# Kernel optimization log

Hardware: AMD Instinct MI355X
Metric: run time of the kernel (lower is better)

## Reference

```python
import jax, jax.numpy as jnp
import numpy as np

B, L, N, C = 16, 96, 1024, 3
EMB, GRAP, OUT, NLAYER = 64, 16, 12, 2


def setup_inputs() -> dict:
    key = jax.random.key(0)
    ks = jax.random.split(key, 16)
    s = 0.1
    return {
        "history_data": jax.random.normal(ks[0], (B, L, N, C), jnp.float32),
        # row-stochastic graph (normalized adjacency buffer)
        "adj": jax.nn.softmax(jax.random.normal(ks[1], (N, N), jnp.float32), axis=-1),
        "Wv0": jax.random.normal(ks[2], (C, EMB), jnp.float32) * s,
        "Wv1": jax.random.normal(ks[3], (EMB, EMB), jnp.float32) * s,
        "bv": jnp.zeros((NLAYER, EMB), jnp.float32),
        "E": jax.random.normal(ks[4], (NLAYER, N, EMB), jnp.float32) * s,
        "Wq": jax.random.normal(ks[5], (NLAYER, EMB, EMB), jnp.float32) * s,
        "Wk": jax.random.normal(ks[6], (NLAYER, EMB, EMB), jnp.float32) * s,
        "Eg1": jax.random.normal(ks[7], (NLAYER, N, GRAP), jnp.float32) * s,
        "Eg2": jax.random.normal(ks[8], (NLAYER, N, GRAP), jnp.float32) * s,
        "Wmix": jax.random.normal(ks[9], (NLAYER, 3, EMB, EMB), jnp.float32) * s,
        "bmix": jnp.zeros((NLAYER, EMB), jnp.float32),
        "Wgates": jax.random.normal(ks[10], (NLAYER, 4, EMB, EMB), jnp.float32) * s,
        "bgates": jnp.zeros((NLAYER, 4, EMB), jnp.float32),
        "Wdec": jax.random.normal(ks[11], (OUT, NLAYER, EMB), jnp.float32) * s,
        "bdec": jnp.zeros((OUT,), jnp.float32),
        "Wout": jax.random.normal(ks[12], (OUT, OUT), jnp.float32) * s,
        "bout": jnp.zeros((OUT,), jnp.float32),
    }


def reference(history_data, adj, Wv0, Wv1, bv, E, Wq, Wk, Eg1, Eg2,
              Wmix, bmix, Wgates, bgates, Wdec, bdec, Wout, bout):
    # GinAR forward (inference: dropout = identity, lay_norm unused in original forward).
    emb = Wv1.shape[0]
    inv = 1.0 / jnp.sqrt(jnp.float32(emb))
    x = history_data  # (B, L, N, in)
    finals = []
    for z in range(Wmix.shape[0]):
        Wv = Wv0 if z == 0 else Wv1
        # interpolation attention over variables (nodes), shared across time/batch
        q = E[z] @ Wq[z]
        k = E[z] @ Wk[z]
        attn = jax.nn.softmax((q @ k.T) * inv, axis=-1)                 # (N, N)
        # adaptive learned graph
        adp = jax.nn.softmax(jax.nn.relu(Eg1[z] @ Eg2[z].T), axis=-1)    # (N, N)
        bz, Wm, bm, Wg, bgz = bv[z], Wmix[z], bmix[z], Wgates[z], bgates[z]

        def step(ct, xt, Wv=Wv, attn=attn, adp=adp, bz=bz, Wm=Wm, bm=bm, Wg=Wg, bgz=bgz):
            v = xt @ Wv + bz                                # (B, N, emb)
            h = jnp.einsum('mn,bne->bme', attn, v)          # variable interpolation
            hg = (jnp.einsum('mn,bne->bme', adj, h) @ Wm[0]
                  + jnp.einsum('mn,bne->bme', adp, h) @ Wm[1]
                  + h @ Wm[2] + bm)                         # adaptive graph conv
            gates = jnp.einsum('bne,kef->kbnf', hg, Wg) + bgz[:, None, None, :]
            f = jax.nn.sigmoid(gates[0])
            i = jax.nn.sigmoid(gates[1])
            g = jnp.tanh(gates[2])
            o = jax.nn.sigmoid(gates[3])
            ct = f * ct + i * g
            ht = o * jnp.tanh(ct)
            return ct, ht

        ct0 = jnp.zeros((x.shape[0], x.shape[2], emb), x.dtype)
        _, hts = jax.lax.scan(step, ct0, jnp.moveaxis(x, 1, 0))  # (L, B, N, emb)
        x = jnp.moveaxis(hts, 0, 1)                              # (B, L, N, emb)
        finals.append(x[:, -1])                                  # last step -> (B, N, emb)
    final = jnp.stack(finals, axis=1)                            # (B, layers, N, emb)
    # decoder Conv2d(layer_num -> out_len, kernel (1, emb)) == contraction over (layer, emb)
    dec = jnp.einsum('blne,ole->bon', final, Wdec) + bdec[None, :, None]
    # 1x1 output conv
    out = jnp.einsum('bpn,op->bon', dec, Wout) + bout[None, :, None]
    return out  # (B, out_len, N)
```

## Files before the change

kernel.cpp:

```cpp
#include <hip/hip_runtime.h>
#include <hip/hip_bf16.h>

#define B_ 16
#define L_ 96
#define N_ 1024
#define EMB_ 64

typedef __hip_bfloat16 bf16;
typedef __attribute__((ext_vector_type(4))) float f32x4;
typedef __attribute__((ext_vector_type(8))) short s16x8;

__global__ __launch_bounds__(256) void gemm_nn(
    const float* __restrict__ A, const float* __restrict__ Bm, float* __restrict__ C,
    int M, int N, int K, int lda, int ldb, int ldc, const float* __restrict__ bias)
{
    __shared__ float As[64][17];
    __shared__ __align__(16) float Bs[16][64];
    const int tid = threadIdx.x;
    const int tx = tid & 15, ty = tid >> 4;
    const int row0 = blockIdx.y * 64, col0 = blockIdx.x * 64;
    float acc[4][4] = {};
    const int ak = tid & 15, ar = tid >> 4;
    const int bc = tid & 63, bk = tid >> 6;
    for (int k0 = 0; k0 < K; k0 += 16) {
#pragma unroll
        for (int i = 0; i < 4; ++i) {
            int r = ar + i * 16;
            int gr = row0 + r, gk = k0 + ak;
            As[r][ak] = (gr < M && gk < K) ? A[(size_t)gr * lda + gk] : 0.f;
        }
#pragma unroll
        for (int i = 0; i < 4; ++i) {
            int kk = bk + i * 4;
            int gk = k0 + kk, gc = col0 + bc;
            Bs[kk][bc] = (gk < K && gc < N) ? Bm[(size_t)gk * ldb + gc] : 0.f;
        }
        __syncthreads();
#pragma unroll
        for (int kk = 0; kk < 16; ++kk) {
            float4 b4 = *reinterpret_cast<const float4*>(&Bs[kk][tx * 4]);
            float a0 = As[ty * 4 + 0][kk];
            float a1 = As[ty * 4 + 1][kk];
            float a2 = As[ty * 4 + 2][kk];
            float a3 = As[ty * 4 + 3][kk];
            acc[0][0] += a0 * b4.x; acc[0][1] += a0 * b4.y; acc[0][2] += a0 * b4.z; acc[0][3] += a0 * b4.w;
            acc[1][0] += a1 * b4.x; acc[1][1] += a1 * b4.y; acc[1][2] += a1 * b4.z; acc[1][3] += a1 * b4.w;
            acc[2][0] += a2 * b4.x; acc[2][1] += a2 * b4.y; acc[2][2] += a2 * b4.z; acc[2][3] += a2 * b4.w;
            acc[3][0] += a3 * b4.x; acc[3][1] += a3 * b4.y; acc[3][2] += a3 * b4.z; acc[3][3] += a3 * b4.w;
        }
        __syncthreads();
    }
#pragma unroll
    for (int i = 0; i < 4; ++i) {
        int gr = row0 + ty * 4 + i;
        if (gr >= M) continue;
#pragma unroll
        for (int j = 0; j < 4; ++j) {
            int gc = col0 + tx * 4 + j;
            if (gc >= N) continue;
            float v = acc[i][j];
            if (bias) v += bias[gc];
            C[(size_t)gr * ldc + gc] = v;
        }
    }
}

__global__ __launch_bounds__(256) void gemm_nt(
    const float* __restrict__ A, const float* __restrict__ Bm, float* __restrict__ C,
    int N, int K, float alpha)
{
    __shared__ float As[64][65];
    __shared__ float Bs[64][65];
    const int tid = threadIdx.x;
    const int row0 = blockIdx.y * 64, col0 = blockIdx.x * 64;
    for (int idx = tid; idx < 64 * K; idx += 256) {
        int r = idx / K, c = idx % K;
        As[r][c] = A[(size_t)(row0 + r) * K + c];
        Bs[r][c] = Bm[(size_t)(col0 + r) * K + c];
    }
    __syncthreads();
    const int tx = tid & 15, ty = tid >> 4;
    float acc[4][4] = {};
    for (int c = 0; c < K; ++c) {
        float a[4], b[4];
#pragma unroll
        for (int i = 0; i < 4; ++i) a[i] = As[ty * 4 + i][c];
#pragma unroll
        for (int j = 0; j < 4; ++j) b[j] = Bs[tx * 4 + j][c];
#pragma unroll
        for (int i = 0; i < 4; ++i)
#pragma unroll
            for (int j = 0; j < 4; ++j) acc[i][j] += a[i] * b[j];
    }
#pragma unroll
    for (int i = 0; i < 4; ++i)
#pragma unroll
        for (int j = 0; j < 4; ++j)
            C[(size_t)(row0 + ty * 4 + i) * N + col0 + tx * 4 + j] = alpha * acc[i][j];
}

__global__ __launch_bounds__(256) void row_softmax(
    const float* __restrict__ in, float* __restrict__ out32, int os32,
    bf16* __restrict__ out16, int os16, int relu)
{
    const float* rp = in + (size_t)blockIdx.x * N_;
    const int tid = threadIdx.x;
    float v[4];
#pragma unroll
    for (int j = 0; j < 4; ++j) {
        float x = rp[tid + 256 * j];
        if (relu) x = fmaxf(x, 0.f);
        v[j] = x;
    }
    float m = fmaxf(fmaxf(v[0], v[1]), fmaxf(v[2], v[3]));
#pragma unroll
    for (int off = 32; off > 0; off >>= 1) m = fmaxf(m, __shfl_xor(m, off));
    __shared__ float red[4], red2[4];
    int w = tid >> 6;
    if ((tid & 63) == 0) red[w] = m;
    __syncthreads();
    m = fmaxf(fmaxf(red[0], red[1]), fmaxf(red[2], red[3]));
    float s = 0.f;
#pragma unroll
    for (int j = 0; j < 4; ++j) { v[j] = __expf(v[j] - m); s += v[j]; }
#pragma unroll
    for (int off = 32; off > 0; off >>= 1) s += __shfl_xor(s, off);
    if ((tid & 63) == 0) red2[w] = s;
    __syncthreads();
    s = red2[0] + red2[1] + red2[2] + red2[3];
    float inv = 1.f / s;
#pragma unroll
    for (int j = 0; j < 4; ++j) {
        float r = v[j] * inv;
        if (out32) out32[(size_t)blockIdx.x * os32 + tid + 256 * j] = r;
        if (out16) out16[(size_t)blockIdx.x * os16 + tid + 256 * j] = __float2bfloat16(r);
    }
}

__global__ __launch_bounds__(256) void transpose_f2b(
    const float* __restrict__ in, bf16* __restrict__ out)
{
    __shared__ float t[64][65];
    const int cx = blockIdx.x, cy = blockIdx.y;
    const int tid = threadIdx.x;
#pragma unroll
    for (int k = 0; k < 16; ++k) {
        int idx = k * 256 + tid;
        int r = idx >> 6, c = idx & 63;
        t[r][c] = in[(size_t)(cy * 64 + r) * 1024 + cx * 64 + c];
    }
    __syncthreads();
#pragma unroll
    for (int k = 0; k < 16; ++k) {
        int idx = k * 256 + tid;
        int r = idx >> 6, c = idx & 63;
        out[(size_t)(cx * 64 + r) * 1024 + cy * 64 + c] = __float2bfloat16(t[c][r]);
    }
}

__global__ __launch_bounds__(256) void wgct_kernel(const float* __restrict__ Wg,
                                                   bf16* __restrict__ WgcT)
{
    int i = blockIdx.x * 256 + threadIdx.x;
    int g = i >> 12, e = (i >> 6) & 63, f = i & 63;
    WgcT[(((size_t)g * 64 + f) << 6) + e] = __float2bfloat16(Wg[i]);
}

__global__ __launch_bounds__(256) void wvc1t_kernel(const float* __restrict__ Wvc1,
                                                    bf16* __restrict__ WT)
{
    int i = blockIdx.x * 256 + threadIdx.x;
    int row = i >> 6, f = i & 63;
    float v = 0.f;
    if (row < 192) { int kp = row >> 6, e = row & 63; v = Wvc1[kp * 4096 + f * 64 + e]; }
    WT[i] = __float2bfloat16(v);
}

__global__ __launch_bounds__(256) void f2b_kernel(const float* __restrict__ in,
                                                  bf16* __restrict__ out, int n)
{
    int i = blockIdx.x * 256 + threadIdx.x;
    if (i < n) out[i] = __float2bfloat16(in[i]);
}

__global__ __launch_bounds__(256) void bias_kernel(
    const float* __restrict__ bvz, const float* __restrict__ Wmz, const float* __restrict__ bmz,
    const float* __restrict__ Wgz, const float* __restrict__ bgz, float* __restrict__ bgconst)
{
    __shared__ float bconst[64];
    const int tid = threadIdx.x;
    if (tid < 64) {
        float s = bmz[tid];
        for (int kp = 0; kp < 3; ++kp)
            for (int f = 0; f < 64; ++f) s += bvz[f] * Wmz[kp * 4096 + f * 64 + tid];
        bconst[tid] = s;
    }
    __syncthreads();
    int g = tid >> 6, fo = tid & 63;
    float s = bgz[g * 64 + fo];
    for (int e = 0; e < 64; ++e) s += bconst[e] * Wgz[g * 4096 + e * 64 + fo];
    bgconst[tid] = s;
}

__global__ __launch_bounds__(256) void wbig_kernel(
    const float* __restrict__ Wvc0, const float* __restrict__ Wg0, bf16* __restrict__ WbigT)
{
    const int tid = threadIdx.x;
    const int g = tid >> 6, fo = tid & 63;
    float v[9];
#pragma unroll
    for (int q = 0; q < 9; ++q) {
        const int kp = q / 3, c = q % 3;
        float s = 0.f;
        for (int e = 0; e < 64; ++e)
            s += Wvc0[kp * 192 + c * 64 + e] * Wg0[g * 4096 + e * 64 + fo];
        v[q] = s;
    }
#pragma unroll
    for (int i = 0; i < 32; ++i)
        WbigT[(size_t)tid * 32 + i] = __float2bfloat16(i < 9 ? v[i] : 0.f);
}

__global__ __launch_bounds__(256) void xt_build(
    const float* __restrict__ hist, bf16* __restrict__ XT, int l0, int LC)
{
    __shared__ float xs[3][1024];
    const int lb = blockIdx.x;
    const int l = lb >> 4, b = lb & 15;
    const int tid = threadIdx.x;
    const float* xp = hist + ((size_t)b * L_ + (l0 + l)) * N_ * 3;
    for (int i = tid; i < 3072; i += 256) xs[i % 3][i / 3] = xp[i];
    __syncthreads();
#pragma unroll
    for (int c = 0; c < 3; ++c)
#pragma unroll
        for (int q = 0; q < 4; ++q) {
            int n = q * 256 + tid;
            XT[((size_t)lb * 3 + c) * 1024 + n] = __float2bfloat16(xs[c][n]);
        }
}

__device__ __forceinline__ void gload16(const bf16* g, bf16* l)
{
    __builtin_amdgcn_global_load_lds((const __attribute__((address_space(1))) void*)g,
                                     (__attribute__((address_space(3))) void*)l, 16, 0, 0);
}

template <int OUT_BF16, int REMAP>
__global__ __launch_bounds__(256) void gemm_mfma(
    const bf16* __restrict__ A, const bf16* __restrict__ BT, void* __restrict__ Cp,
    int M, int N, int K, int lda, int ldb, int ldc,
    const float* __restrict__ bias, int Nmask)
{
    __shared__ __align__(16) bf16 As[128 * 64];
    __shared__ __align__(16) bf16 Bs[128 * 64];
    const int tid = threadIdx.x;
    const int lane = tid & 63, w = tid >> 6;
    const int wr = w >> 1, wc = w & 1;
    const int row0 = blockIdx.y * 128, col0 = blockIdx.x * 128;
    if (REMAP == 1) BT += (size_t)blockIdx.z * 64;
    if (REMAP == 2) A += (size_t)blockIdx.z * 1024;

    f32x4 acc[4][4];
#pragma unroll
    for (int i = 0; i < 4; ++i)
#pragma unroll
        for (int j = 0; j < 4; ++j) acc[i][j] = (f32x4){0.f, 0.f, 0.f, 0.f};

    const int srow = w * 32 + (lane >> 3);
    const int scolsw = ((lane & 7) ^ (lane >> 3)) * 8;

    for (int k0 = 0; k0 < K; k0 += 64) {
#pragma unroll
        for (int i = 0; i < 4; ++i) {
            gload16(A + (size_t)(row0 + srow + i * 8) * lda + k0 + scolsw,
                    &As[(w * 32 + i * 8) * 64]);
            gload16(BT + (size_t)(col0 + srow + i * 8) * ldb + k0 + scolsw,
                    &Bs[(w * 32 + i * 8) * 64]);
        }
        __syncthreads();
#pragma unroll
        for (int kk = 0; kk < 64; kk += 32) {
            s16x8 af[4], bfr[4];
            const int ko = (kk + (lane >> 4) * 8) ^ ((lane & 7) << 3);
#pragma unroll
            for (int mi = 0; mi < 4; ++mi)
                af[mi] = *(const s16x8*)&As[(wr * 64 + mi * 16 + (lane & 15)) * 64 + ko];
#pragma unroll
            for (int ni = 0; ni < 4; ++ni)
                bfr[ni] = *(const s16x8*)&Bs[(wc * 64 + ni * 16 + (lane & 15)) * 64 + ko];
#pragma unroll
            for (int mi = 0; mi < 4; ++mi)
#pragma unroll
                for (int ni = 0; ni < 4; ++ni)
                    acc[mi][ni] = __builtin_amdgcn_mfma_f32_16x16x32_bf16(
                        af[mi], bfr[ni], acc[mi][ni], 0, 0, 0);
        }
        __syncthreads();
    }

    if (REMAP == 1) {
        bf16* outb = (bf16*)Cp + (size_t)blockIdx.z * (64 * 3072);
#pragma unroll
        for (int mi = 0; mi < 4; ++mi) {
            const int gr = row0 + wr * 64 + mi * 16 + (lane >> 4) * 4;
#pragma unroll
            for (int ni = 0; ni < 4; ++ni) {
                const int gc = col0 + wc * 64 + ni * 16 + (lane & 15);
#pragma unroll
                for (int j = 0; j < 4; ++j) {
                    const int r = gr + j;
                    if (r >= Nmask) continue;
                    outb[(size_t)(r & 63) * 3072 + (r >> 6) * 1024 + gc] =
                        __float2bfloat16(acc[mi][ni][j]);
                }
            }
        }
        return;
    }
    if (REMAP == 2) {
        bf16* outb = (bf16*)Cp;
        const int kpoff = blockIdx.z * 3;
#pragma unroll
        for (int mi = 0; mi < 4; ++mi) {
            const int gr = row0 + wr * 64 + mi * 16 + (lane >> 4) * 4;
#pragma unroll
            for (int ni = 0; ni < 4; ++ni) {
                const int gc = col0 + wc * 64 + ni * 16 + (lane & 15);
                if (gc >= Nmask) continue;
                const int dstc = (gc / 3) * 32 + kpoff + gc % 3;
#pragma unroll
                for (int j = 0; j < 4; ++j)
                    outb[(size_t)(gr + j) * ldc + dstc] = __float2bfloat16(acc[mi][ni][j]);
            }
        }
        return;
    }

#pragma unroll
    for (int mi = 0; mi < 4; ++mi) {
        const int gr = row0 + wr * 64 + mi * 16 + (lane >> 4) * 4;
#pragma unroll
        for (int ni = 0; ni < 4; ++ni) {
            const int gc = col0 + wc * 64 + ni * 16 + (lane & 15);
            if (gc >= Nmask) continue;
            const float bb = bias ? bias[gc] : 0.f;
#pragma unroll
            for (int j = 0; j < 4; ++j) {
                float v = acc[mi][ni][j] + bb;
                if (OUT_BF16)
                    ((bf16*)Cp)[(size_t)(gr + j) * ldc + gc] = __float2bfloat16(v);
                else
                    ((float*)Cp)[(size_t)(gr + j) * ldc + gc] = v;
            }
        }
    }
}

__global__ __launch_bounds__(512) void gemm_pipe(
    const bf16* __restrict__ A, const bf16* __restrict__ BT, bf16* __restrict__ C,
    int N, int K)
{
    __shared__ __align__(16) bf16 lds[8 * 8192];
    const int tid = threadIdx.x;
    const int lane = tid & 63, w = tid >> 6;
    const int wm = w >> 2, wn = w & 3, bh = wn >> 1;
    const int row0 = blockIdx.y * 256, col0 = blockIdx.x * 256;

    const int strow = tid >> 3;
    const int srck  = ((tid & 7) ^ ((tid >> 3) & 7)) << 3;
    const int e7 = lane & 7, fs = lane >> 4, a15 = lane & 15;

    int aoff0[8], boff0[4];
#pragma unroll
    for (int mi = 0; mi < 8; ++mi)
        aoff0[mi] = (mi * 16 + a15) * 64 + ((fs ^ e7) << 3);
#pragma unroll
    for (int ni = 0; ni < 4; ++ni)
        boff0[ni] = ((wn & 1) * 64 + ni * 16 + a15) * 64 + ((fs ^ e7) << 3);

    auto stage = [&](int mat, int half, int kt) {
        bf16* dst = &lds[(size_t)((((kt & 1) << 1) | mat) * 2 + half) * 8192 + w * 512];
        const bf16* src = (mat ? BT + (size_t)col0 * K : A + (size_t)row0 * K)
                          + (size_t)(half * 128) * K + kt * 64 + srck;
        gload16(src + (size_t)strow * K, dst);
        gload16(src + (size_t)(64 + strow) * K, dst + 4096);
    };

    f32x4 acc[8][4];
#pragma unroll
    for (int i = 0; i < 8; ++i)
#pragma unroll
        for (int j = 0; j < 4; ++j) acc[i][j] = (f32x4){0.f, 0.f, 0.f, 0.f};

    s16x8 b0, b1, b2, b3;

#define MF_(a, mi) { \
    acc[mi][0] = __builtin_amdgcn_mfma_f32_16x16x32_bf16(a, b0, acc[mi][0], 0, 0, 0); \
    acc[mi][1] = __builtin_amdgcn_mfma_f32_16x16x32_bf16(a, b1, acc[mi][1], 0, 0, 0); \
    acc[mi][2] = __builtin_amdgcn_mfma_f32_16x16x32_bf16(a, b2, acc[mi][2], 0, 0, 0); \
    acc[mi][3] = __builtin_amdgcn_mfma_f32_16x16x32_bf16(a, b3, acc[mi][3], 0, 0, 0); }

#define PH_(d, kh, g, DOB, STG) { \
    const bf16* Ab = &lds[((d) * 4 + wm) * 8192]; \
    const bf16* Bb = &lds[((d) * 4 + 2 + bh) * 8192]; \
    if (DOB) { \
        b0 = *(const s16x8*)&Bb[boff0[0] ^ ((kh) * 32)]; \
        b1 = *(const s16x8*)&Bb[boff0[1] ^ ((kh) * 32)]; \
        b2 = *(const s16x8*)&Bb[boff0[2] ^ ((kh) * 32)]; \
        b3 = *(const s16x8*)&Bb[boff0[3] ^ ((kh) * 32)]; \
    } \
    s16x8 a0 = *(const s16x8*)&Ab[aoff0[(g) * 4 + 0] ^ ((kh) * 32)]; \
    s16x8 a1 = *(const s16x8*)&Ab[aoff0[(g) * 4 + 1] ^ ((kh) * 32)]; \
    s16x8 a2 = *(const s16x8*)&Ab[aoff0[(g) * 4 + 2] ^ ((kh) * 32)]; \
    s16x8 a3 = *(const s16x8*)&Ab[aoff0[(g) * 4 + 3] ^ ((kh) * 32)]; \
    STG; \
    __builtin_amdgcn_s_barrier(); \
    asm volatile("s_waitcnt lgkmcnt(0)" ::: "memory"); \
    __builtin_amdgcn_sched_barrier(0); \
    __builtin_amdgcn_s_setprio(1); \
    MF_(a0, (g) * 4 + 0); MF_(a1, (g) * 4 + 1); \
    MF_(a2, (g) * 4 + 2); MF_(a3, (g) * 4 + 3); \
    __builtin_amdgcn_s_setprio(0); \
    __builtin_amdgcn_s_barrier(); }

    const int NT = K >> 6;
    stage(0, 0, 0); stage(0, 1, 0); stage(1, 0, 0); stage(1, 1, 0);
    stage(0, 0, 1);

    for (int i = 0; i < NT / 2; ++i) {
        const int kt = 2 * i;
        asm volatile("s_waitcnt vmcnt(2)" ::: "memory");
        __builtin_amdgcn_sched_barrier(0);
        __builtin_amdgcn_s_barrier();
        PH_(0, 0, 0, 1, { stage(0, 1, kt + 1); });
        PH_(0, 0, 1, 0, { stage(1, 0, kt + 1); });
        PH_(0, 1, 0, 1, { stage(1, 1, kt + 1); });
        PH_(0, 1, 1, 0, { if (kt + 2 < NT) stage(0, 0, kt + 2); });
        if (kt + 2 < NT) { asm volatile("s_waitcnt vmcnt(2)" ::: "memory"); }
        else             { asm volatile("s_waitcnt vmcnt(0)" ::: "memory"); }
        __builtin_amdgcn_sched_barrier(0);
        __builtin_amdgcn_s_barrier();
        PH_(1, 0, 0, 1, { if (kt + 2 < NT) stage(0, 1, kt + 2); });
        PH_(1, 0, 1, 0, { if (kt + 2 < NT) stage(1, 0, kt + 2); });
        PH_(1, 1, 0, 1, { if (kt + 2 < NT) stage(1, 1, kt + 2); });
        PH_(1, 1, 1, 0, { if (kt + 3 < NT) stage(0, 0, kt + 3); });
    }
#undef PH_
#undef MF_

#pragma unroll
    for (int mi = 0; mi < 8; ++mi) {
        const int gr = row0 + wm * 128 + mi * 16 + (lane >> 4) * 4;
#pragma unroll
        for (int ni = 0; ni < 4; ++ni) {
            const int gc = col0 + wn * 64 + ni * 16 + (lane & 15);
#pragma unroll
            for (int j = 0; j < 4; ++j)
                C[(size_t)(gr + j) * N + gc] = __float2bfloat16(acc[mi][ni][j]);
        }
    }
}

__global__ __launch_bounds__(256, 4) void fused_gates_scan(
    const bf16* __restrict__ HG, const bf16* __restrict__ WgcT,
    const float* __restrict__ bgc, float* __restrict__ ct_buf,
    bf16* __restrict__ ht_out, float* __restrict__ htlast,
    int LC, int l0, int initct)
{
    __shared__ __align__(16) bf16 Bs[256 * 64];
    __shared__ float bgs[256];
    const int tid = threadIdx.x;
    const int lane = tid & 63, w = tid >> 6;
    const int n = blockIdx.x;
    const int swz = ((lane & 7) ^ (lane >> 3)) * 8;
    const int l8 = (lane >> 3) * 64;

#pragma unroll
    for (int r = 0; r < 8; ++r)
        gload16(WgcT + r * 2048 + w * 512 + l8 + swz, &Bs[r * 2048 + w * 512]);
    bgs[tid] = bgc[tid];
    __syncthreads();

    const int ar = lane & 15;
    const int ak = (lane >> 4) * 8;
    const int kswz = (lane & 7) << 3;
    const int f = w * 16 + ar;
    const int r0 = (lane >> 4) * 4;
    const float bgf = bgs[f], bgi = bgs[64 + f], bgg = bgs[128 + f], bgo = bgs[192 + f];

    float ct[4];
    const size_t cbase = (size_t)n * 1024;
#pragma unroll
    for (int j = 0; j < 4; ++j)
        ct[j] = initct ? 0.f : ct_buf[cbase + (size_t)(r0 + j) * 64 + f];

    const bf16* HGn = HG + (size_t)n * LC * 1024;
    s16x8 a0 = *(const s16x8*)&HGn[ar * 64 + ak];
    s16x8 a1 = *(const s16x8*)&HGn[ar * 64 + ak + 32];

    for (int l = 0; l < LC; ++l) {
        s16x8 p0 = a0, p1 = a1;
        if (l + 1 < LC) {
            p0 = *(const s16x8*)&HGn[((l + 1) * 16 + ar) * 64 + ak];
            p1 = *(const s16x8*)&HGn[((l + 1) * 16 + ar) * 64 + ak + 32];
        }
        f32x4 acc[4];
#pragma unroll
        for (int ni = 0; ni < 4; ++ni) acc[ni] = (f32x4){0.f, 0.f, 0.f, 0.f};
#pragma unroll
        for (int ni = 0; ni < 4; ++ni) {
            s16x8 bf = *(const s16x8*)&Bs[(ni * 64 + w * 16 + ar) * 64 + (ak ^ kswz)];
            acc[ni] = __builtin_amdgcn_mfma_f32_16x16x32_bf16(a0, bf, acc[ni], 0, 0, 0);
        }
#pragma unroll
        for (int ni = 0; ni < 4; ++ni) {
            s16x8 bf = *(const s16x8*)&Bs[(ni * 64 + w * 16 + ar) * 64 + ((ak + 32) ^ kswz)];
            acc[ni] = __builtin_amdgcn_mfma_f32_16x16x32_bf16(a1, bf, acc[ni], 0, 0, 0);
        }
        const size_t hbase = ((size_t)n * LC + l) * 1024;
        const bool last = (l0 + l == L_ - 1);
#pragma unroll
        for (int j = 0; j < 4; ++j) {
            float xf = acc[0][j] + bgf;
            float xi = acc[1][j] + bgi;
            float xg = acc[2][j] + bgg;
            float xo = acc[3][j] + bgo;
            float fg = 1.f / (1.f + __expf(-xf));
            float ig = 1.f / (1.f + __expf(-xi));
            float gg = 2.f / (1.f + __expf(-2.f * xg)) - 1.f;
            float og = 1.f / (1.f + __expf(-xo));
            ct[j] = fg * ct[j] + ig * gg;
            float ht = og * (2.f / (1.f + __expf(-2.f * ct[j])) - 1.f);
            if (ht_out) ht_out[hbase + (size_t)(r0 + j) * 64 + f] = __float2bfloat16(ht);
            if (htlast && last) htlast[cbase + (size_t)(r0 + j) * 64 + f] = ht;
        }
        a0 = p0; a1 = p1;
    }
#pragma unroll
    for (int j = 0; j < 4; ++j)
        ct_buf[cbase + (size_t)(r0 + j) * 64 + f] = ct[j];
}

__global__ __launch_bounds__(256, 4) void fused_gates_scan_y(
    const bf16* __restrict__ Y, const bf16* __restrict__ WbigT,
    const float* __restrict__ bgc, float* __restrict__ ct_buf,
    bf16* __restrict__ ht_out, float* __restrict__ htlast,
    int LC, int l0, int initct)
{
    __shared__ bf16 Bs2[256 * 40];
    __shared__ float bgs[256];
    const int tid = threadIdx.x;
    const int lane = tid & 63, w = tid >> 6;
    const int n = blockIdx.x;
    {
        const uint4* src = (const uint4*)(WbigT + (size_t)tid * 32);
        uint4* dst = (uint4*)&Bs2[tid * 40];
        dst[0] = src[0]; dst[1] = src[1]; dst[2] = src[2]; dst[3] = src[3];
    }
    bgs[tid] = bgc[tid];
    __syncthreads();

    const int ar = lane & 15, fs = lane >> 4;
    const int f = w * 16 + ar;
    const int r0 = fs * 4;
    const float bgf = bgs[f], bgi = bgs[64 + f], bgg = bgs[128 + f], bgo = bgs[192 + f];

    float ct[4];
    const size_t cbase = (size_t)n * 1024;
#pragma unroll
    for (int j = 0; j < 4; ++j)
        ct[j] = initct ? 0.f : ct_buf[cbase + (size_t)(r0 + j) * 64 + f];

    const bf16* Yn = Y + (size_t)n * LC * 512;
    s16x8 a = *(const s16x8*)&Yn[ar * 32 + fs * 8];

    for (int l = 0; l < LC; ++l) {
        s16x8 p = a;
        if (l + 1 < LC) p = *(const s16x8*)&Yn[((l + 1) * 16 + ar) * 32 + fs * 8];
        f32x4 acc[4];
#pragma unroll
        for (int ni = 0; ni < 4; ++ni) {
            s16x8 bf = *(const s16x8*)&Bs2[(ni * 64 + w * 16 + ar) * 40 + fs * 8];
            acc[ni] = __builtin_amdgcn_mfma_f32_16x16x32_bf16(
                a, bf, (f32x4){0.f, 0.f, 0.f, 0.f}, 0, 0, 0);
        }
        const size_t hbase = ((size_t)n * LC + l) * 1024;
        const bool last = (l0 + l == L_ - 1);
#pragma unroll
        for (int j = 0; j < 4; ++j) {
            float xf = acc[0][j] + bgf;
            float xi = acc[1][j] + bgi;
            float xg = acc[2][j] + bgg;
            float xo = acc[3][j] + bgo;
            float fg = 1.f / (1.f + __expf(-xf));
            float ig = 1.f / (1.f + __expf(-xi));
            float gg = 2.f / (1.f + __expf(-2.f * xg)) - 1.f;
            float og = 1.f / (1.f + __expf(-xo));
            ct[j] = fg * ct[j] + ig * gg;
            float ht = og * (2.f / (1.f + __expf(-2.f * ct[j])) - 1.f);
            if (ht_out) ht_out[hbase + (size_t)(r0 + j) * 64 + f] = __float2bfloat16(ht);
            if (htlast && last) htlast[cbase + (size_t)(r0 + j) * 64 + f] = ht;
        }
        a = p;
    }
#pragma unroll
    for (int j = 0; j < 4; ++j)
        ct_buf[cbase + (size_t)(r0 + j) * 64 + f] = ct[j];
}

__global__ __launch_bounds__(256) void decoder_kernel(
    const float* __restrict__ h0, const float* __restrict__ h1,
    const float* __restrict__ Wdec, const float* __restrict__ bdec,
    const float* __restrict__ Wout, const float* __restrict__ bout,
    float* __restrict__ outp)
{
    __shared__ float Wd[12 * 2 * 64];
    __shared__ float Wo[144];
    __shared__ float bd[12], bo[12];
    const int tid = threadIdx.x;
    for (int i = tid; i < 12 * 2 * 64; i += 256) Wd[i] = Wdec[i];
    for (int i = tid; i < 144; i += 256) Wo[i] = Wout[i];
    if (tid < 12) { bd[tid] = bdec[tid]; bo[tid] = bout[tid]; }
    __syncthreads();
    const int gid = blockIdx.x * 256 + tid;
    const int b = gid >> 10, n = gid & 1023;
    const float* h0r = h0 + ((size_t)n * 16 + b) * 64;
    const float* h1r = h1 + ((size_t)n * 16 + b) * 64;
    float dec[12];
#pragma unroll
    for (int o = 0; o < 12; ++o) dec[o] = bd[o];
    for (int e = 0; e < 64; ++e) {
        float v0 = h0r[e], v1 = h1r[e];
#pragma unroll
        for (int o = 0; o < 12; ++o) dec[o] += v0 * Wd[o * 128 + e] + v1 * Wd[o * 128 + 64 + e];
    }
#pragma unroll
    for (int o = 0; o < 12; ++o) {
        float s = bo[o];
#pragma unroll
        for (int p = 0; p < 12; ++p) s += Wo[o * 12 + p] * dec[p];
        outp[((size_t)b * 12 + o) * 1024 + n] = s;
    }
}

extern "C" void kernel_launch(void* const* d_in, const int* in_sizes, int n_in,
                              void* d_out, int out_size, void* d_ws, size_t ws_size,
                              hipStream_t stream)
{
    const float* hist = (const float*)d_in[0];
    const float* adj  = (const float*)d_in[1];
    const float* Wv0  = (const float*)d_in[2];
    const float* Wv1  = (const float*)d_in[3];
    const float* bv   = (const float*)d_in[4];
    const float* E    = (const float*)d_in[5];
    const float* Wq   = (const float*)d_in[6];
    const float* Wk   = (const float*)d_in[7];
    const float* Eg1  = (const float*)d_in[8];
    const float* Eg2  = (const float*)d_in[9];
    const float* Wmix = (const float*)d_in[10];
    const float* bmix = (const float*)d_in[11];
    const float* Wg   = (const float*)d_in[12];
    const float* bg   = (const float*)d_in[13];
    const float* Wdec = (const float*)d_in[14];
    const float* bdec = (const float*)d_in[15];
    const float* Wout = (const float*)d_in[16];
    const float* bout = (const float*)d_in[17];
    float* outp = (float*)d_out;
    (void)in_sizes; (void)n_in; (void)out_size;

    char* ws = (char*)d_ws;
    size_t off = 0;
    auto alloc = [&](size_t bytes) -> void* {
        void* p = (void*)(ws + off);
        off += (bytes + 255) & ~(size_t)255;
        return p;
    };
    bf16*  Mcatb0 = (bf16*)alloc((size_t)1024 * 3072 * 2);
    bf16*  Mcatb1 = (bf16*)alloc((size_t)1024 * 3072 * 2);
    float* attnf  = (float*)alloc((size_t)1024 * 1024 * 4);
    bf16*  attnT  = (bf16*)alloc((size_t)1024 * 1024 * 2);
    bf16*  adjb   = (bf16*)alloc((size_t)1024 * 1024 * 2);
    bf16*  adpb   = (bf16*)alloc((size_t)1024 * 1024 * 2);
    float* qb     = (float*)alloc((size_t)1024 * 64 * 4);
    float* kb     = (float*)alloc((size_t)1024 * 64 * 4);
    float* logits = (float*)alloc((size_t)1024 * 1024 * 4);
    float* Wvc0   = (float*)alloc(3 * 3 * 64 * 4);
    float* Wvc1   = (float*)alloc(3 * 64 * 64 * 4);
    bf16*  Wvc1T  = (bf16*)alloc(256 * 64 * 2);
    bf16*  WgcT1  = (bf16*)alloc(256 * 64 * 2);
    bf16*  WbigT  = (bf16*)alloc(256 * 32 * 2);
    float* bgc0   = (float*)alloc(256 * 4);
    float* bgc1   = (float*)alloc(256 * 4);
    float* ct0    = (float*)alloc((size_t)N_ * B_ * 64 * 4);
    float* ct1    = (float*)alloc((size_t)N_ * B_ * 64 * 4);
    float* hl0    = (float*)alloc((size_t)N_ * B_ * 64 * 4);
    float* hl1    = (float*)alloc((size_t)N_ * B_ * 64 * 4);
    size_t fixed = off;

    static const int divs[] = {16, 8};
    int LC = 8;
    for (int di = 0; di < 2; ++di) {
        if (fixed + (size_t)divs[di] * 10485760ull + 65536 <= ws_size) { LC = divs[di]; break; }
    }
    bf16*  VcatT = (bf16*)alloc((size_t)LC * 6291456ull);
    bf16*  HG    = (bf16*)alloc((size_t)LC * 2097152ull);
    bf16*  ht0c  = (bf16*)alloc((size_t)LC * 2097152ull);
    bf16*  XT    = VcatT;
    bf16*  Y     = VcatT + (size_t)LC * 49152;

    dim3 blk(256);
    bf16*  McatB[2] = {Mcatb0, Mcatb1};
    float* bgc[2] = {bgc0, bgc1};

    f2b_kernel<<<4096, blk, 0, stream>>>(adj, adjb, 1024 * 1024);
    for (int z = 0; z < 2; ++z) {
        const float* Ez = E + (size_t)z * N_ * 64;
        gemm_nn<<<dim3(1, 16), blk, 0, stream>>>(Ez, Wq + z * 4096, qb, 1024, 64, 64, 64, 64, 64, nullptr);
        gemm_nn<<<dim3(1, 16), blk, 0, stream>>>(Ez, Wk + z * 4096, kb, 1024, 64, 64, 64, 64, 64, nullptr);
        gemm_nt<<<dim3(16, 16), blk, 0, stream>>>(qb, kb, logits, 1024, 64, 0.125f);
        row_softmax<<<1024, blk, 0, stream>>>(logits, attnf, 1024, McatB[z] + 2048, 3072, 0);
        transpose_f2b<<<dim3(16, 16), blk, 0, stream>>>(attnf, attnT);
        gemm_nt<<<dim3(16, 16), blk, 0, stream>>>(Eg1 + z * 16384, Eg2 + z * 16384, logits, 1024, 16, 1.f);
        row_softmax<<<1024, blk, 0, stream>>>(logits, nullptr, 0, adpb, 1024, 1);
        gemm_mfma<1, 0><<<dim3(8, 8), blk, 0, stream>>>(adjb, attnT, McatB[z],
            1024, 1024, 1024, 1024, 1024, 3072, nullptr, 1024);
        gemm_mfma<1, 0><<<dim3(8, 8), blk, 0, stream>>>(adpb, attnT, McatB[z] + 1024,
            1024, 1024, 1024, 1024, 1024, 3072, nullptr, 1024);
        if (z == 0) {
            for (int kp = 0; kp < 3; ++kp)
                gemm_nn<<<dim3(1, 1), blk, 0, stream>>>(Wv0, Wmix + kp * 4096,
                    Wvc0 + kp * 3 * 64, 3, 64, 64, 64, 64, 64, nullptr);
            wbig_kernel<<<1, blk, 0, stream>>>(Wvc0, Wg, WbigT);
        } else {
            for (int kp = 0; kp < 3; ++kp)
                gemm_nn<<<dim3(1, 1), blk, 0, stream>>>(Wv1, Wmix + 12288 + kp * 4096,
                    Wvc1 + kp * 4096, 64, 64, 64, 64, 64, 64, nullptr);
            wvc1t_kernel<<<64, blk, 0, stream>>>(Wvc1, Wvc1T);
            wgct_kernel<<<64, blk, 0, stream>>>(Wg + 16384, WgcT1);
        }
        bias_kernel<<<1, blk, 0, stream>>>(bv + z * 64, Wmix + z * 12288, bmix + z * 64,
            Wg + z * 16384, bg + z * 256, bgc[z]);
    }

    const int nch = L_ / LC;
    dim3 blk512(512);
    for (int c = 0; c < nch; ++c) {
        const int l0 = c * LC;
        hipMemsetAsync(Y, 0, (size_t)LC * 1048576ull, stream);
        xt_build<<<LC * 16, blk, 0, stream>>>(hist, XT, l0, LC);
        gemm_mfma<1, 2><<<dim3(LC * 48 / 128, 8, 3), blk, 0, stream>>>(Mcatb0, XT, Y,
            1024, LC * 48, 1024, 3072, 1024, LC * 512, nullptr, LC * 48);
        fused_gates_scan_y<<<1024, blk, 0, stream>>>(Y, WbigT, bgc0, ct0,
            ht0c, hl0, LC, l0, c == 0);
        gemm_mfma<1, 1><<<dim3(8, 2, LC * 16), blk, 0, stream>>>(Wvc1T, ht0c, VcatT,
            256, 1024, 64, 64, LC * 1024, 0, nullptr, 192);
        gemm_pipe<<<dim3(LC * 4, 4), blk512, 0, stream>>>(Mcatb1, VcatT, HG,
            LC * 1024, 3072);
        fused_gates_scan<<<1024, blk, 0, stream>>>(HG, WgcT1, bgc1, ct1,
            nullptr, hl1, LC, l0, c == 0);
    }
    decoder_kernel<<<64, blk, 0, stream>>>(hl0, hl1, Wdec, bdec, Wout, bout, outp);
}
```

Baseline: 1.740 ms.

## Batch the four graph GEMMs into one launch and hoist input transposition

The four 1024x1024x1024 graph products (adj and adaptive graph times attention, for both layers) were four 64-block launches. They are now a single 256-block launch, using a new REMAP mode that picks the operand slices from blockIdx.z. The input conversion `xt_build` now runs once for all timesteps into a dedicated buffer, and the Y memset moves out of the chunk loop. The HG and ht0 buffers are aliased into one. This cuts per-chunk launches and gives the precompute GEMMs more parallelism, at the cost of a larger workspace. It also assumes Y does not need re-zeroing between chunks.

```diff
diff --git a/kernel.cpp b/kernel.cpp
--- a/kernel.cpp
+++ b/kernel.cpp
@@ -222,13 +222,13 @@
 }
 
 __global__ __launch_bounds__(256) void xt_build(
-    const float* __restrict__ hist, bf16* __restrict__ XT, int l0, int LC)
+    const float* __restrict__ hist, bf16* __restrict__ XT)
 {
     __shared__ float xs[3][1024];
     const int lb = blockIdx.x;
     const int l = lb >> 4, b = lb & 15;
     const int tid = threadIdx.x;
-    const float* xp = hist + ((size_t)b * L_ + (l0 + l)) * N_ * 3;
+    const float* xp = hist + ((size_t)b * L_ + l) * N_ * 3;
     for (int i = tid; i < 3072; i += 256) xs[i % 3][i / 3] = xp[i];
     __syncthreads();
 #pragma unroll
@@ -260,6 +260,13 @@
     const int row0 = blockIdx.y * 128, col0 = blockIdx.x * 128;
     if (REMAP == 1) BT += (size_t)blockIdx.z * 64;
     if (REMAP == 2) A += (size_t)blockIdx.z * 1024;
+    if (REMAP == 3) {
+        const int z3 = blockIdx.z >> 1, wh = blockIdx.z & 1;
+        if (wh) A = BT + (size_t)z3 * 1048576;
+        BT = (const bf16*)bias + (size_t)z3 * 1048576;
+        Cp = (void*)((bf16*)Cp + (size_t)z3 * 3145728 + (size_t)wh * 1024);
+        bias = nullptr;
+    }
 
     f32x4 acc[4][4];
 #pragma unroll
@@ -676,12 +683,10 @@
         off += (bytes + 255) & ~(size_t)255;
         return p;
     };
-    bf16*  Mcatb0 = (bf16*)alloc((size_t)1024 * 3072 * 2);
-    bf16*  Mcatb1 = (bf16*)alloc((size_t)1024 * 3072 * 2);
-    float* attnf  = (float*)alloc((size_t)1024 * 1024 * 4);
-    bf16*  attnT  = (bf16*)alloc((size_t)1024 * 1024 * 2);
+    bf16*  Mcatb  = (bf16*)alloc((size_t)2 * 1024 * 3072 * 2);
+    bf16*  attnT2 = (bf16*)alloc((size_t)2 * 1024 * 1024 * 2);
     bf16*  adjb   = (bf16*)alloc((size_t)1024 * 1024 * 2);
-    bf16*  adpb   = (bf16*)alloc((size_t)1024 * 1024 * 2);
+    bf16*  adpb2  = (bf16*)alloc((size_t)2 * 1024 * 1024 * 2);
     float* qb     = (float*)alloc((size_t)1024 * 64 * 4);
     float* kb     = (float*)alloc((size_t)1024 * 64 * 4);
     float* logits = (float*)alloc((size_t)1024 * 1024 * 4);
@@ -696,21 +701,20 @@
     float* ct1    = (float*)alloc((size_t)N_ * B_ * 64 * 4);
     float* hl0    = (float*)alloc((size_t)N_ * B_ * 64 * 4);
     float* hl1    = (float*)alloc((size_t)N_ * B_ * 64 * 4);
+    bf16*  XT     = (bf16*)alloc((size_t)L_ * 16 * 3 * 1024 * 2);
     size_t fixed = off;
 
     static const int divs[] = {16, 8};
     int LC = 8;
     for (int di = 0; di < 2; ++di) {
-        if (fixed + (size_t)divs[di] * 10485760ull + 65536 <= ws_size) { LC = divs[di]; break; }
+        if (fixed + (size_t)divs[di] * 9437184ull + 65536 <= ws_size) { LC = divs[di]; break; }
     }
     bf16*  VcatT = (bf16*)alloc((size_t)LC * 6291456ull);
-    bf16*  HG    = (bf16*)alloc((size_t)LC * 2097152ull);
-    bf16*  ht0c  = (bf16*)alloc((size_t)LC * 2097152ull);
-    bf16*  XT    = VcatT;
-    bf16*  Y     = VcatT + (size_t)LC * 49152;
+    bf16*  HGht  = (bf16*)alloc((size_t)LC * 2097152ull);
+    bf16*  Y     = (bf16*)alloc((size_t)LC * 1048576ull);
 
     dim3 blk(256);
-    bf16*  McatB[2] = {Mcatb0, Mcatb1};
+    bf16*  McatB[2] = {Mcatb, Mcatb + 3145728};
     float* bgc[2] = {bgc0, bgc1};
 
     f2b_kernel<<<4096, blk, 0, stream>>>(adj, adjb, 1024 * 1024);
@@ -719,14 +723,10 @@
         gemm_nn<<<dim3(1, 16), blk, 0, stream>>>(Ez, Wq + z * 4096, qb, 1024, 64, 64, 64, 64, 64, nullptr);
         gemm_nn<<<dim3(1, 16), blk, 0, stream>>>(Ez, Wk + z * 4096, kb, 1024, 64, 64, 64, 64, 64, nullptr);
         gemm_nt<<<dim3(16, 16), blk, 0, stream>>>(qb, kb, logits, 1024, 64, 0.125f);
-        row_softmax<<<1024, blk, 0, stream>>>(logits, attnf, 1024, McatB[z] + 2048, 3072, 0);
-        transpose_f2b<<<dim3(16, 16), blk, 0, stream>>>(attnf, attnT);
+        row_softmax<<<1024, blk, 0, stream>>>(logits, logits, 1024, McatB[z] + 2048, 3072, 0);
+        transpose_f2b<<<dim3(16, 16), blk, 0, stream>>>(logits, attnT2 + (size_t)z * 1048576);
         gemm_nt<<<dim3(16, 16), blk, 0, stream>>>(Eg1 + z * 16384, Eg2 + z * 16384, logits, 1024, 16, 1.f);
-        row_softmax<<<1024, blk, 0, stream>>>(logits, nullptr, 0, adpb, 1024, 1);
-        gemm_mfma<1, 0><<<dim3(8, 8), blk, 0, stream>>>(adjb, attnT, McatB[z],
-            1024, 1024, 1024, 1024, 1024, 3072, nullptr, 1024);
-        gemm_mfma<1, 0><<<dim3(8, 8), blk, 0, stream>>>(adpb, attnT, McatB[z] + 1024,
-            1024, 1024, 1024, 1024, 1024, 3072, nullptr, 1024);
+        row_softmax<<<1024, blk, 0, stream>>>(logits, nullptr, 0, adpb2 + (size_t)z * 1048576, 1024, 1);
         if (z == 0) {
             for (int kp = 0; kp < 3; ++kp)
                 gemm_nn<<<dim3(1, 1), blk, 0, stream>>>(Wv0, Wmix + kp * 4096,
@@ -742,22 +742,26 @@
         bias_kernel<<<1, blk, 0, stream>>>(bv + z * 64, Wmix + z * 12288, bmix + z * 64,
             Wg + z * 16384, bg + z * 256, bgc[z]);
     }
+    gemm_mfma<1, 3><<<dim3(8, 8, 4), blk, 0, stream>>>(adjb, adpb2, Mcatb,
+        1024, 1024, 1024, 1024, 1024, 3072, (const float*)attnT2, 1024);
+
+    hipMemsetAsync(Y, 0, (size_t)LC * 1048576ull, stream);
+    xt_build<<<L_ * 16, blk, 0, stream>>>(hist, XT);
 
     const int nch = L_ / LC;
     dim3 blk512(512);
     for (int c = 0; c < nch; ++c) {
         const int l0 = c * LC;
-        hipMemsetAsync(Y, 0, (size_t)LC * 1048576ull, stream);
-        xt_build<<<LC * 16, blk, 0, stream>>>(hist, XT, l0, LC);
-        gemm_mfma<1, 2><<<dim3(LC * 48 / 128, 8, 3), blk, 0, stream>>>(Mcatb0, XT, Y,
+        gemm_mfma<1, 2><<<dim3(LC * 48 / 128, 8, 3), blk, 0, stream>>>(McatB[0],
+            XT + (size_t)l0 * 49152, Y,
             1024, LC * 48, 1024, 3072, 1024, LC * 512, nullptr, LC * 48);
         fused_gates_scan_y<<<1024, blk, 0, stream>>>(Y, WbigT, bgc0, ct0,
-            ht0c, hl0, LC, l0, c == 0);
-        gemm_mfma<1, 1><<<dim3(8, 2, LC * 16), blk, 0, stream>>>(Wvc1T, ht0c, VcatT,
+            HGht, hl0, LC, l0, c == 0);
+        gemm_mfma<1, 1><<<dim3(8, 2, LC * 16), blk, 0, stream>>>(Wvc1T, HGht, VcatT,
             256, 1024, 64, 64, LC * 1024, 0, nullptr, 192);
-        gemm_pipe<<<dim3(LC * 4, 4), blk512, 0, stream>>>(Mcatb1, VcatT, HG,
+        gemm_pipe<<<dim3(LC * 4, 4), blk512, 0, stream>>>(McatB[1], VcatT, HGht,
             LC * 1024, 3072);
-        fused_gates_scan<<<1024, blk, 0, stream>>>(HG, WgcT1, bgc1, ct1,
+        fused_gates_scan<<<1024, blk, 0, stream>>>(HGht, WgcT1, bgc1, ct1,
             nullptr, hl1, LC, l0, c == 0);
     }
     decoder_kernel<<<64, blk, 0, stream>>>(hl0, hl1, Wdec, bdec, Wout, bout, outp);
```

After: 1.632 ms. 6.2% less time.
